# Kernel tuning notes

Hardware: AMD Instinct MI355X
Metric: run time of the kernel (lower is better)

The kernel has to match this reference:

```python
import jax, jax.numpy as jnp
import numpy as np

NUM_HEADS = 5
TEMP = 0.3
NEG_FILL = -1e-7  # note: NOT -inf; masked entries still contribute ~exp(0) to softmax, faithful to torch code


def setup_inputs() -> dict:
    key = jax.random.key(0)
    k1, k2, k3, k4, k5 = jax.random.split(key, 5)
    B, N, F_IN, F_OUT = 8, 1024, 320, 320
    h = jax.random.normal(k1, (B, N, F_IN), dtype=jnp.float32)
    Wqk = jax.random.normal(k2, (F_IN, 2 * F_IN), dtype=jnp.float32) * (1.0 / np.sqrt(F_IN))
    bqk = jax.random.normal(k3, (2 * F_IN,), dtype=jnp.float32) * 0.01
    weight = jax.random.normal(k4, (F_IN, F_OUT), dtype=jnp.float32) * (1.0 / np.sqrt(F_OUT))
    bias = jax.random.normal(k5, (F_OUT,), dtype=jnp.float32) * 0.01
    return {"h": h, "Wqk": Wqk, "bqk": bqk, "weight": weight, "bias": bias}


def reference(h, Wqk, bqk, weight, bias):
    B, N, F = h.shape
    H = NUM_HEADS
    D = F // H
    # linear -> [b, n, 2F]; einops 'b n (h d qk)' => reshape (b, n, h, d, 2)
    qk = (h @ Wqk + bqk).reshape(B, N, H, D, 2)
    q = jnp.transpose(qk[..., 0], (0, 2, 1, 3))  # b h n d
    k = jnp.transpose(qk[..., 1], (0, 2, 1, 3))  # b h n d
    scale = D ** -0.5
    dots = jnp.einsum('bhqd,bhkd->bhqk', q, k) * scale  # b h n n
    at = dots.sum(axis=1)  # b n n  (sum over heads)
    # sort-based threshold: keep values >= descending-sorted value at index N//6
    thr = jax.lax.top_k(at, N // 6 + 1)[0][..., -1]  # b n
    adj = jnp.where(at < thr[:, :, None], jnp.asarray(NEG_FILL, at.dtype), at)
    attn = jax.nn.softmax(adj / TEMP, axis=2)  # b n n
    out_feature = jnp.einsum('bij,bjd->bid', attn, h)  # values = raw input h
    return out_feature @ weight + bias
```

## Files before the change

### kernel.cpp

```cpp
#include <hip/hip_runtime.h>
#include <hip/hip_fp16.h>


typedef __attribute__((ext_vector_type(8))) _Float16 half8;
typedef __attribute__((ext_vector_type(4))) float f32x4;

__device__ __forceinline__ void stage_tile(const __half* g, __half* lds,
                                           int nrow16, int ld, int wave, int lane) {
    const int r = lane >> 2;
    const int c = ((lane & 3) ^ ((lane >> 3) & 3)) * 8;
    for (int i = wave; i < nrow16; i += 4) {
        const __half* src = g + (long)(i * 16 + r) * ld + c;
        __builtin_amdgcn_global_load_lds(
            (const __attribute__((address_space(1))) unsigned int*)src,
            (__attribute__((address_space(3))) unsigned int*)(lds + i * 512),
            16, 0, 0);
    }
}

template <int WM, int WN, int EPI>
__global__ __launch_bounds__(256) void gemm_nt(
    const __half* __restrict__ A, const __half* __restrict__ B,
    void* __restrict__ C, void* __restrict__ C2,
    const float* __restrict__ bias,
    int K, int lda, int ldb, int ldc,
    long sA, long sB, long sC, float alpha)
{
    constexpr int BM = WM * 64;
    constexpr int BN = WN * 64;
    constexpr int BUF = BM * 32 + BN * 32;
    __shared__ __half smem[2 * BUF];

    const int tid  = threadIdx.x;
    const int lane = tid & 63;
    const int wave = tid >> 6;
    const int wm   = wave / WN;
    const int wn   = wave % WN;
    const int bz   = blockIdx.z;

    const __half* Ab = A + bz * sA + (long)blockIdx.y * BM * lda;
    const __half* Bb = B + bz * sB + (long)blockIdx.x * BN * ldb;

    f32x4 acc[4][4];
    #pragma unroll
    for (int i = 0; i < 4; ++i)
        #pragma unroll
        for (int j = 0; j < 4; ++j) acc[i][j] = (f32x4){0.f, 0.f, 0.f, 0.f};

    const int lrow = lane & 15;
    const int quad = lane >> 4;
    const int swz = (quad ^ ((lrow >> 1) & 3)) * 8;

    const int nIter = K >> 5;

    stage_tile(Ab, smem, BM / 16, lda, wave, lane);
    stage_tile(Bb, smem + BM * 32, BN / 16, ldb, wave, lane);

    for (int it = 0; it < nIter; ++it) {
        __syncthreads();

        if (it + 1 < nIter) {
            __half* nb = smem + ((it + 1) & 1) * BUF;
            const int k1 = (it + 1) << 5;
            stage_tile(Ab + k1, nb, BM / 16, lda, wave, lane);
            stage_tile(Bb + k1, nb + BM * 32, BN / 16, ldb, wave, lane);
        }

        const __half* buf = smem + (it & 1) * BUF;
        const __half* pA = buf + (wm * 64 + lrow) * 32 + swz;
        const __half* pB = buf + BM * 32 + (wn * 64 + lrow) * 32 + swz;
        half8 ah[4], bh[4];
        #pragma unroll
        for (int mt = 0; mt < 4; ++mt) ah[mt] = *(const half8*)(pA + mt * 512);
        #pragma unroll
        for (int nt = 0; nt < 4; ++nt) bh[nt] = *(const half8*)(pB + nt * 512);
        #pragma unroll
        for (int mt = 0; mt < 4; ++mt)
            #pragma unroll
            for (int nt = 0; nt < 4; ++nt)
                acc[mt][nt] = __builtin_amdgcn_mfma_f32_16x16x32_f16(
                    ah[mt], bh[nt], acc[mt][nt], 0, 0, 0);
    }

    const int row_base = blockIdx.y * BM + wm * 64;
    const int col_base = blockIdx.x * BN + wn * 64;
    #pragma unroll
    for (int mt = 0; mt < 4; ++mt)
        #pragma unroll
        for (int nt = 0; nt < 4; ++nt)
            #pragma unroll
            for (int r = 0; r < 4; ++r) {
                const int row = row_base + mt * 16 + quad * 4 + r;
                const int col = col_base + nt * 16 + lrow;
                const float v = acc[mt][nt][r];
                if (EPI == 1) {
                    const float val = v + bias[col];
                    const long idx = (long)row * 320 + (col >> 1);
                    if (col & 1) ((__half*)C2)[idx] = __float2half(val);
                    else         ((__half*)C)[idx]  = __float2half(val);
                } else if (EPI == 2) {
                    ((__half*)C)[(long)row * ldc + col] = __float2half(v);
                } else if (EPI == 3) {
                    ((float*)C)[bz * sC + (long)row * ldc + col] = v + bias[col];
                } else {
                    ((__half*)C)[bz * sC + (long)row * ldc + col] =
                        __float2half(alpha * v);
                }
            }
}

__global__ __launch_bounds__(256) void prep_all(
    const float* __restrict__ h, ushort4* __restrict__ h16,
    const float* __restrict__ Wqk, __half* __restrict__ WqkT,
    const float* __restrict__ weight, __half* __restrict__ wTp)
{
    const int bx = blockIdx.x;
    if (bx < 2560) {
        const int i = bx * 256 + threadIdx.x;
        const float4 v = ((const float4*)h)[i];
        ushort4 o;
        o.x = __half_as_ushort(__float2half(v.x));
        o.y = __half_as_ushort(__float2half(v.y));
        o.z = __half_as_ushort(__float2half(v.z));
        o.w = __half_as_ushort(__float2half(v.w));
        h16[i] = o;
        return;
    }
    __shared__ float t[32][33];
    const float* src;
    __half* dst;
    int ldS, ldT, c0, r0;
    if (bx < 2760) {
        const int b = bx - 2560;
        src = Wqk; dst = WqkT; ldS = 640; ldT = 320;
        c0 = (b % 20) * 32; r0 = (b / 20) * 32;
    } else {
        const int b = bx - 2760;
        src = weight; dst = wTp; ldS = 320; ldT = 320;
        c0 = (b % 10) * 32; r0 = (b / 10) * 32;
    }
    const int lx = threadIdx.x & 31, ly = threadIdx.x >> 5;
    #pragma unroll
    for (int i = 0; i < 4; ++i)
        t[ly + 8 * i][lx] = src[(long)(r0 + ly + 8 * i) * ldS + c0 + lx];
    __syncthreads();
    #pragma unroll
    for (int i = 0; i < 4; ++i)
        dst[(long)(c0 + ly + 8 * i) * ldT + r0 + lx] = __float2half(t[lx][ly + 8 * i]);
}

__global__ __launch_bounds__(256) void topk_softmax(const __half* __restrict__ at,
                                                    __half* __restrict__ attn)
{
    __shared__ int hist[4][256];
    const int lane = threadIdx.x & 63;
    const int wave = threadIdx.x >> 6;
    const long row = (long)blockIdx.x * 4 + wave;

    unsigned short vs[16];
    {
        const uint4* p = (const uint4*)(at + row * 1024 + lane * 16);
        *(uint4*)&vs[0] = p[0];
        *(uint4*)&vs[8] = p[1];
    }

    unsigned key[16];
    #pragma unroll
    for (int i = 0; i < 16; ++i) {
        const unsigned u = vs[i];
        key[i] = (u & 0x8000u) ? ((~u) & 0xFFFFu) : (u | 0x8000u);
    }

    unsigned prefix = 0, pmask = 0;
    int kk = 171;

    #pragma unroll
    for (int pass = 0; pass < 2; ++pass) {
        const int shift = 8 - 8 * pass;
        *(int4*)&hist[wave][lane * 4] = make_int4(0, 0, 0, 0);
        __syncthreads();
        #pragma unroll
        for (int i = 0; i < 16; ++i) {
            if ((key[i] & pmask) == prefix)
                atomicAdd(&hist[wave][(key[i] >> shift) & 255], 1);
        }
        __syncthreads();
        const int4 hh = *(const int4*)&hist[wave][lane * 4];
        const int s = hh.x + hh.y + hh.z + hh.w;
        int suf = s;
        #pragma unroll
        for (int off = 1; off < 64; off <<= 1) {
            const int o = __shfl_down(suf, off);
            if (lane + off < 64) suf += o;
        }
        const int cgt3 = suf - s;
        const int cgt2 = cgt3 + hh.w;
        const int cgt1 = cgt2 + hh.z;
        const int cgt0 = cgt1 + hh.y;
        int pick = 0x7FFFFFFF;
        if (cgt3 < kk && kk <= cgt3 + hh.w) pick = ((4 * lane + 3) << 16) | (kk - cgt3);
        if (cgt2 < kk && kk <= cgt2 + hh.z) pick = ((4 * lane + 2) << 16) | (kk - cgt2);
        if (cgt1 < kk && kk <= cgt1 + hh.y) pick = ((4 * lane + 1) << 16) | (kk - cgt1);
        if (cgt0 < kk && kk <= cgt0 + hh.x) pick = ((4 * lane + 0) << 16) | (kk - cgt0);
        #pragma unroll
        for (int off = 32; off > 0; off >>= 1) pick = min(pick, __shfl_xor(pick, off));
        const unsigned digit = (unsigned)(pick >> 16);
        kk = pick & 0xFFFF;
        prefix |= digit << shift;
        pmask  |= 0xFFu << shift;
        if (pass == 0) __syncthreads();
    }

    const unsigned short tu = (prefix & 0x8000u) ? (unsigned short)(prefix & 0x7FFFu)
                                                 : (unsigned short)((~prefix) & 0xFFFFu);
    const float thr = __half2float(__ushort_as_half(tu));

    float lg[16];
    float mx = -3.4e38f;
    #pragma unroll
    for (int i = 0; i < 16; ++i) {
        const float v = __half2float(__ushort_as_half(vs[i]));
        const float a = (v < thr) ? -1e-7f : v;
        lg[i] = a * (1.0f / 0.3f);
        mx = fmaxf(mx, lg[i]);
    }
    #pragma unroll
    for (int off = 32; off > 0; off >>= 1) mx = fmaxf(mx, __shfl_xor(mx, off));

    float e[16];
    float sum = 0.f;
    #pragma unroll
    for (int i = 0; i < 16; ++i) { e[i] = __expf(lg[i] - mx); sum += e[i]; }
    #pragma unroll
    for (int off = 32; off > 0; off >>= 1) sum += __shfl_xor(sum, off);
    const float inv = 1.0f / sum;

    unsigned short os[16];
    #pragma unroll
    for (int i = 0; i < 16; ++i) os[i] = __half_as_ushort(__float2half(e[i] * inv));
    uint4* q = (uint4*)(attn + row * 1024 + lane * 16);
    q[0] = *(const uint4*)&os[0];
    q[1] = *(const uint4*)&os[8];
}

extern "C" void kernel_launch(void* const* d_in, const int* in_sizes, int n_in,
                              void* d_out, int out_size, void* d_ws, size_t ws_size,
                              hipStream_t stream) {
    (void)in_sizes; (void)n_in; (void)out_size; (void)ws_size;

    const float* h      = (const float*)d_in[0];
    const float* Wqk    = (const float*)d_in[1];
    const float* bqk    = (const float*)d_in[2];
    const float* weight = (const float*)d_in[3];
    const float* bias   = (const float*)d_in[4];
    float* out = (float*)d_out;

    char* p = (char*)d_ws;
    __half* at   = (__half*)p; p += 8388608L * 2;
    __half* attn = (__half*)p; p += 8388608L * 2;
    __half* h16  = (__half*)p; p += 2621440L * 2;
    __half* Q    = (__half*)p; p += 2621440L * 2;
    __half* Kb   = (__half*)p; p += 2621440L * 2;
    __half* WqkT = (__half*)p; p += 640L * 320 * 2;
    __half* wTp  = (__half*)p; p += 384L * 320 * 2;
    __half* hWT  = (__half*)p; p += 384L * 8192 * 2;

    prep_all<<<2860, 256, 0, stream>>>(h, (ushort4*)h16, Wqk, WqkT, weight, wTp);

    gemm_nt<2, 2, 2><<<dim3(64, 3, 1), 256, 0, stream>>>(
        wTp, h16, hWT, nullptr, nullptr,
        320, 320, 320, 8192, 0, 0, 0, 1.0f);

    gemm_nt<4, 1, 1><<<dim3(10, 32, 1), 256, 0, stream>>>(
        h16, WqkT, Q, Kb, bqk,
        320, 320, 320, 0, 0, 0, 0, 1.0f);

    gemm_nt<2, 2, 4><<<dim3(8, 8, 8), 256, 0, stream>>>(
        Q, Kb, at, nullptr, nullptr,
        320, 320, 320, 1024, 327680, 327680, 1048576, 0.125f);

    topk_softmax<<<2048, 256, 0, stream>>>(at, attn);

    gemm_nt<4, 1, 3><<<dim3(5, 4, 8), 256, 0, stream>>>(
        attn, hWT, out, nullptr, bias,
        1024, 1024, 8192, 320, 1048576, 1024, 327680, 1.0f);
}
```

Baseline: 146.0 us.

## Fuse QK^T, top-k softmax, and attn@hW into one per-row-block kernel

```diff
diff --git a/kernel.cpp b/kernel.cpp
--- a/kernel.cpp
+++ b/kernel.cpp
@@ -4,6 +4,8 @@
 
 typedef __attribute__((ext_vector_type(8))) _Float16 half8;
 typedef __attribute__((ext_vector_type(4))) float f32x4;
+
+#define ATP 1056
 
 __device__ __forceinline__ void stage_tile(const __half* g, __half* lds,
                                            int nrow16, int ld, int wave, int lane) {
@@ -18,28 +20,21 @@
     }
 }
 
-template <int WM, int WN, int EPI>
-__global__ __launch_bounds__(256) void gemm_nt(
+template <int EPI>
+__device__ __forceinline__ void gemm_body(
     const __half* __restrict__ A, const __half* __restrict__ B,
-    void* __restrict__ C, void* __restrict__ C2,
-    const float* __restrict__ bias,
-    int K, int lda, int ldb, int ldc,
-    long sA, long sB, long sC, float alpha)
+    void* __restrict__ C, void* __restrict__ C2, const float* __restrict__ bias,
+    int lda, int ldb, int ldc, int bx, int by, __half* smem)
 {
-    constexpr int BM = WM * 64;
-    constexpr int BN = WN * 64;
-    constexpr int BUF = BM * 32 + BN * 32;
-    __shared__ __half smem[2 * BUF];
-
+    constexpr int BUF = 8192;
     const int tid  = threadIdx.x;
     const int lane = tid & 63;
     const int wave = tid >> 6;
-    const int wm   = wave / WN;
-    const int wn   = wave % WN;
-    const int bz   = blockIdx.z;
-
-    const __half* Ab = A + bz * sA + (long)blockIdx.y * BM * lda;
-    const __half* Bb = B + bz * sB + (long)blockIdx.x * BN * ldb;
+    const int wm   = wave >> 1;
+    const int wn   = wave & 1;
+
+    const __half* Ab = A + (long)by * 128 * lda;
+    const __half* Bb = B + (long)bx * 128 * ldb;
 
     f32x4 acc[4][4];
     #pragma unroll
@@ -51,24 +46,19 @@
     const int quad = lane >> 4;
     const int swz = (quad ^ ((lrow >> 1) & 3)) * 8;
 
-    const int nIter = K >> 5;
-
-    stage_tile(Ab, smem, BM / 16, lda, wave, lane);
-    stage_tile(Bb, smem + BM * 32, BN / 16, ldb, wave, lane);
-
-    for (int it = 0; it < nIter; ++it) {
+    stage_tile(Ab, smem, 8, lda, wave, lane);
+    stage_tile(Bb, smem + 4096, 8, ldb, wave, lane);
+
+    for (int it = 0; it < 10; ++it) {
         __syncthreads();
-
-        if (it + 1 < nIter) {
+        if (it + 1 < 10) {
             __half* nb = smem + ((it + 1) & 1) * BUF;
-            const int k1 = (it + 1) << 5;
-            stage_tile(Ab + k1, nb, BM / 16, lda, wave, lane);
-            stage_tile(Bb + k1, nb + BM * 32, BN / 16, ldb, wave, lane);
-        }
-
+            stage_tile(Ab + (it + 1) * 32, nb, 8, lda, wave, lane);
+            stage_tile(Bb + (it + 1) * 32, nb + 4096, 8, ldb, wave, lane);
+        }
         const __half* buf = smem + (it & 1) * BUF;
         const __half* pA = buf + (wm * 64 + lrow) * 32 + swz;
-        const __half* pB = buf + BM * 32 + (wn * 64 + lrow) * 32 + swz;
+        const __half* pB = buf + 4096 + (wn * 64 + lrow) * 32 + swz;
         half8 ah[4], bh[4];
         #pragma unroll
         for (int mt = 0; mt < 4; ++mt) ah[mt] = *(const half8*)(pA + mt * 512);
@@ -82,8 +72,8 @@
                     ah[mt], bh[nt], acc[mt][nt], 0, 0, 0);
     }
 
-    const int row_base = blockIdx.y * BM + wm * 64;
-    const int col_base = blockIdx.x * BN + wn * 64;
+    const int row_base = by * 128 + wm * 64;
+    const int col_base = bx * 128 + wn * 64;
     #pragma unroll
     for (int mt = 0; mt < 4; ++mt)
         #pragma unroll
@@ -98,15 +88,28 @@
                     const long idx = (long)row * 320 + (col >> 1);
                     if (col & 1) ((__half*)C2)[idx] = __float2half(val);
                     else         ((__half*)C)[idx]  = __float2half(val);
-                } else if (EPI == 2) {
+                } else {
                     ((__half*)C)[(long)row * ldc + col] = __float2half(v);
-                } else if (EPI == 3) {
-                    ((float*)C)[bz * sC + (long)row * ldc + col] = v + bias[col];
-                } else {
-                    ((__half*)C)[bz * sC + (long)row * ldc + col] =
-                        __float2half(alpha * v);
                 }
             }
+}
+
+__global__ __launch_bounds__(256) void g1_combined(
+    const __half* __restrict__ h16, const __half* __restrict__ wTp,
+    const __half* __restrict__ WqkT, __half* __restrict__ hWT,
+    __half* __restrict__ Q, __half* __restrict__ Kb,
+    const float* __restrict__ bqk)
+{
+    __shared__ __half smem[2 * 8192];
+    const int bx = blockIdx.x;
+    if (bx < 192) {
+        gemm_body<2>(wTp, h16, hWT, nullptr, nullptr,
+                     320, 320, 8192, bx % 64, bx / 64, smem);
+    } else {
+        const int b = bx - 192;
+        gemm_body<1>(h16, WqkT, Q, Kb, bqk,
+                     320, 320, 320, b % 5, b / 5, smem);
+    }
 }
 
 __global__ __launch_bounds__(256) void prep_all(
@@ -149,98 +152,208 @@
         dst[(long)(c0 + ly + 8 * i) * ldT + r0 + lx] = __float2half(t[lx][ly + 8 * i]);
 }
 
-__global__ __launch_bounds__(256) void topk_softmax(const __half* __restrict__ at,
-                                                    __half* __restrict__ attn)
+__global__ __launch_bounds__(256) void attn_fused(
+    const __half* __restrict__ Q, const __half* __restrict__ Kmat,
+    const __half* __restrict__ hWT, const float* __restrict__ bias,
+    float* __restrict__ out)
 {
+    __shared__ __half sAT[32 * ATP];
+    __shared__ __half sStg[2 * 10240];
     __shared__ int hist[4][256];
-    const int lane = threadIdx.x & 63;
-    const int wave = threadIdx.x >> 6;
-    const long row = (long)blockIdx.x * 4 + wave;
-
-    unsigned short vs[16];
-    {
-        const uint4* p = (const uint4*)(at + row * 1024 + lane * 16);
-        *(uint4*)&vs[0] = p[0];
-        *(uint4*)&vs[8] = p[1];
-    }
-
-    unsigned key[16];
-    #pragma unroll
-    for (int i = 0; i < 16; ++i) {
-        const unsigned u = vs[i];
-        key[i] = (u & 0x8000u) ? ((~u) & 0xFFFFu) : (u | 0x8000u);
-    }
-
-    unsigned prefix = 0, pmask = 0;
-    int kk = 171;
-
-    #pragma unroll
-    for (int pass = 0; pass < 2; ++pass) {
-        const int shift = 8 - 8 * pass;
-        *(int4*)&hist[wave][lane * 4] = make_int4(0, 0, 0, 0);
+
+    const int tid  = threadIdx.x;
+    const int lane = tid & 63;
+    const int wave = tid >> 6;
+    const int lrow = lane & 15;
+    const int quad = lane >> 4;
+    const int swz  = (quad ^ ((lrow >> 1) & 3)) * 8;
+
+    const int batch = blockIdx.x >> 5;
+    const int r0    = (blockIdx.x & 31) * 32;
+    const __half* Qb = Q    + ((long)batch * 1024 + r0) * 320;
+    const __half* Kb = Kmat + (long)batch * 1024 * 320;
+    const __half* Wb = hWT  + (long)batch * 1024;
+    float* outB = out + ((long)batch * 1024 + r0) * 320;
+
+    for (int cc = 0; cc < 4; ++cc) {
+        const __half* Kcc = Kb + (long)(cc * 256) * 320;
+        stage_tile(Qb, sStg, 2, 320, wave, lane);
+        stage_tile(Kcc, sStg + 1024, 16, 320, wave, lane);
+
+        f32x4 acc[2][4];
+        #pragma unroll
+        for (int i = 0; i < 2; ++i)
+            #pragma unroll
+            for (int j = 0; j < 4; ++j) acc[i][j] = (f32x4){0.f, 0.f, 0.f, 0.f};
+
+        for (int it = 0; it < 10; ++it) {
+            __syncthreads();
+            if (it + 1 < 10) {
+                __half* nb = sStg + ((it + 1) & 1) * 10240;
+                stage_tile(Qb + (it + 1) * 32, nb, 2, 320, wave, lane);
+                stage_tile(Kcc + (it + 1) * 32, nb + 1024, 16, 320, wave, lane);
+            }
+            const __half* buf = sStg + (it & 1) * 10240;
+            half8 qf[2], kf[4];
+            #pragma unroll
+            for (int mt = 0; mt < 2; ++mt)
+                qf[mt] = *(const half8*)(buf + (mt * 16 + lrow) * 32 + swz);
+            #pragma unroll
+            for (int nt = 0; nt < 4; ++nt)
+                kf[nt] = *(const half8*)(buf + 1024 + (wave * 64 + nt * 16 + lrow) * 32 + swz);
+            #pragma unroll
+            for (int mt = 0; mt < 2; ++mt)
+                #pragma unroll
+                for (int nt = 0; nt < 4; ++nt)
+                    acc[mt][nt] = __builtin_amdgcn_mfma_f32_16x16x32_f16(
+                        qf[mt], kf[nt], acc[mt][nt], 0, 0, 0);
+        }
+        #pragma unroll
+        for (int mt = 0; mt < 2; ++mt)
+            #pragma unroll
+            for (int nt = 0; nt < 4; ++nt)
+                #pragma unroll
+                for (int rg = 0; rg < 4; ++rg) {
+                    const int row = mt * 16 + quad * 4 + rg;
+                    const int col = cc * 256 + wave * 64 + nt * 16 + lrow;
+                    const int slot = ((col >> 3) & 3) ^ ((row >> 1) & 3);
+                    sAT[row * ATP + (col >> 5) * 32 + slot * 8 + (col & 7)] =
+                        __float2half(0.125f * acc[mt][nt][rg]);
+                }
+    }
+    __syncthreads();
+
+    for (int rr = 0; rr < 8; ++rr) {
+        const int row = wave * 8 + rr;
+        const int rsw = (row >> 1) & 3;
+        unsigned short vs[16];
+        #pragma unroll
+        for (int j = 0; j < 2; ++j) {
+            const int g = lane * 2 + j;
+            const int addr = row * ATP + (g >> 2) * 32 + ((g & 3) ^ rsw) * 8;
+            *(uint4*)&vs[8 * j] = *(const uint4*)&sAT[addr];
+        }
+
+        unsigned key[16];
+        #pragma unroll
+        for (int i = 0; i < 16; ++i) {
+            const unsigned u = vs[i];
+            key[i] = (u & 0x8000u) ? ((~u) & 0xFFFFu) : (u | 0x8000u);
+        }
+
+        unsigned prefix = 0, pmask = 0;
+        int kk = 171;
+        #pragma unroll
+        for (int pass = 0; pass < 2; ++pass) {
+            const int shift = 8 - 8 * pass;
+            *(int4*)&hist[wave][lane * 4] = make_int4(0, 0, 0, 0);
+            __syncthreads();
+            #pragma unroll
+            for (int i = 0; i < 16; ++i) {
+                if ((key[i] & pmask) == prefix)
+                    atomicAdd(&hist[wave][(key[i] >> shift) & 255], 1);
+            }
+            __syncthreads();
+            const int4 hh = *(const int4*)&hist[wave][lane * 4];
+            const int s = hh.x + hh.y + hh.z + hh.w;
+            int suf = s;
+            #pragma unroll
+            for (int off = 1; off < 64; off <<= 1) {
+                const int o = __shfl_down(suf, off);
+                if (lane + off < 64) suf += o;
+            }
+            const int cgt3 = suf - s;
+            const int cgt2 = cgt3 + hh.w;
+            const int cgt1 = cgt2 + hh.z;
+            const int cgt0 = cgt1 + hh.y;
+            int pick = 0x7FFFFFFF;
+            if (cgt3 < kk && kk <= cgt3 + hh.w) pick = ((4 * lane + 3) << 16) | (kk - cgt3);
+            if (cgt2 < kk && kk <= cgt2 + hh.z) pick = ((4 * lane + 2) << 16) | (kk - cgt2);
+            if (cgt1 < kk && kk <= cgt1 + hh.y) pick = ((4 * lane + 1) << 16) | (kk - cgt1);
+            if (cgt0 < kk && kk <= cgt0 + hh.x) pick = ((4 * lane + 0) << 16) | (kk - cgt0);
+            #pragma unroll
+            for (int off = 32; off > 0; off >>= 1) pick = min(pick, __shfl_xor(pick, off));
+            kk = pick & 0xFFFF;
+            prefix |= ((unsigned)(pick >> 16)) << shift;
+            pmask  |= 0xFFu << shift;
+            if (pass == 0) __syncthreads();
+        }
+
+        const unsigned short tu = (prefix & 0x8000u) ? (unsigned short)(prefix & 0x7FFFu)
+                                                     : (unsigned short)((~prefix) & 0xFFFFu);
+        const float thr = __half2float(__ushort_as_half(tu));
+
+        float lg[16];
+        float mx = -3.4e38f;
+        #pragma unroll
+        for (int i = 0; i < 16; ++i) {
+            const float v = __half2float(__ushort_as_half(vs[i]));
+            const float a = (v < thr) ? -1e-7f : v;
+            lg[i] = a * (1.0f / 0.3f);
+            mx = fmaxf(mx, lg[i]);
+        }
+        #pragma unroll
+        for (int off = 32; off > 0; off >>= 1) mx = fmaxf(mx, __shfl_xor(mx, off));
+
+        float e[16];
+        float sum = 0.f;
+        #pragma unroll
+        for (int i = 0; i < 16; ++i) { e[i] = __expf(lg[i] - mx); sum += e[i]; }
+        #pragma unroll
+        for (int off = 32; off > 0; off >>= 1) sum += __shfl_xor(sum, off);
+        const float inv = 1.0f / sum;
+
+        unsigned short os[16];
+        #pragma unroll
+        for (int i = 0; i < 16; ++i) os[i] = __half_as_ushort(__float2half(e[i] * inv));
+        #pragma unroll
+        for (int j = 0; j < 2; ++j) {
+            const int g = lane * 2 + j;
+            const int addr = row * ATP + (g >> 2) * 32 + ((g & 3) ^ rsw) * 8;
+            *(uint4*)&sAT[addr] = *(const uint4*)&os[8 * j];
+        }
+    }
+    __syncthreads();
+
+    f32x4 acc3[2][5];
+    #pragma unroll
+    for (int i = 0; i < 2; ++i)
+        #pragma unroll
+        for (int j = 0; j < 5; ++j) acc3[i][j] = (f32x4){0.f, 0.f, 0.f, 0.f};
+
+    stage_tile(Wb, sStg, 20, 8192, wave, lane);
+    for (int it = 0; it < 32; ++it) {
         __syncthreads();
-        #pragma unroll
-        for (int i = 0; i < 16; ++i) {
-            if ((key[i] & pmask) == prefix)
-                atomicAdd(&hist[wave][(key[i] >> shift) & 255], 1);
-        }
-        __syncthreads();
-        const int4 hh = *(const int4*)&hist[wave][lane * 4];
-        const int s = hh.x + hh.y + hh.z + hh.w;
-        int suf = s;
-        #pragma unroll
-        for (int off = 1; off < 64; off <<= 1) {
-            const int o = __shfl_down(suf, off);
-            if (lane + off < 64) suf += o;
-        }
-        const int cgt3 = suf - s;
-        const int cgt2 = cgt3 + hh.w;
-        const int cgt1 = cgt2 + hh.z;
-        const int cgt0 = cgt1 + hh.y;
-        int pick = 0x7FFFFFFF;
-        if (cgt3 < kk && kk <= cgt3 + hh.w) pick = ((4 * lane + 3) << 16) | (kk - cgt3);
-        if (cgt2 < kk && kk <= cgt2 + hh.z) pick = ((4 * lane + 2) << 16) | (kk - cgt2);
-        if (cgt1 < kk && kk <= cgt1 + hh.y) pick = ((4 * lane + 1) << 16) | (kk - cgt1);
-        if (cgt0 < kk && kk <= cgt0 + hh.x) pick = ((4 * lane + 0) << 16) | (kk - cgt0);
-        #pragma unroll
-        for (int off = 32; off > 0; off >>= 1) pick = min(pick, __shfl_xor(pick, off));
-        const unsigned digit = (unsigned)(pick >> 16);
-        kk = pick & 0xFFFF;
-        prefix |= digit << shift;
-        pmask  |= 0xFFu << shift;
-        if (pass == 0) __syncthreads();
-    }
-
-    const unsigned short tu = (prefix & 0x8000u) ? (unsigned short)(prefix & 0x7FFFu)
-                                                 : (unsigned short)((~prefix) & 0xFFFFu);
-    const float thr = __half2float(__ushort_as_half(tu));
-
-    float lg[16];
-    float mx = -3.4e38f;
-    #pragma unroll
-    for (int i = 0; i < 16; ++i) {
-        const float v = __half2float(__ushort_as_half(vs[i]));
-        const float a = (v < thr) ? -1e-7f : v;
-        lg[i] = a * (1.0f / 0.3f);
-        mx = fmaxf(mx, lg[i]);
-    }
-    #pragma unroll
-    for (int off = 32; off > 0; off >>= 1) mx = fmaxf(mx, __shfl_xor(mx, off));
-
-    float e[16];
-    float sum = 0.f;
-    #pragma unroll
-    for (int i = 0; i < 16; ++i) { e[i] = __expf(lg[i] - mx); sum += e[i]; }
-    #pragma unroll
-    for (int off = 32; off > 0; off >>= 1) sum += __shfl_xor(sum, off);
-    const float inv = 1.0f / sum;
-
-    unsigned short os[16];
-    #pragma unroll
-    for (int i = 0; i < 16; ++i) os[i] = __half_as_ushort(__float2half(e[i] * inv));
-    uint4* q = (uint4*)(attn + row * 1024 + lane * 16);
-    q[0] = *(const uint4*)&os[0];
-    q[1] = *(const uint4*)&os[8];
+        if (it + 1 < 32)
+            stage_tile(Wb + (it + 1) * 32, sStg + ((it + 1) & 1) * 10240,
+                       20, 8192, wave, lane);
+        const __half* buf = sStg + (it & 1) * 10240;
+        const int k0 = it * 32;
+        half8 af[2], bf[5];
+        #pragma unroll
+        for (int mt = 0; mt < 2; ++mt)
+            af[mt] = *(const half8*)(sAT + (mt * 16 + lrow) * ATP + k0 + swz);
+        #pragma unroll
+        for (int j = 0; j < 5; ++j)
+            bf[j] = *(const half8*)(buf + ((wave * 5 + j) * 16 + lrow) * 32 + swz);
+        #pragma unroll
+        for (int mt = 0; mt < 2; ++mt)
+            #pragma unroll
+            for (int j = 0; j < 5; ++j)
+                acc3[mt][j] = __builtin_amdgcn_mfma_f32_16x16x32_f16(
+                    af[mt], bf[j], acc3[mt][j], 0, 0, 0);
+    }
+
+    #pragma unroll
+    for (int mt = 0; mt < 2; ++mt)
+        #pragma unroll
+        for (int j = 0; j < 5; ++j)
+            #pragma unroll
+            for (int rg = 0; rg < 4; ++rg) {
+                const int row = mt * 16 + quad * 4 + rg;
+                const int col = wave * 80 + j * 16 + lrow;
+                outB[(long)row * 320 + col] = acc3[mt][j][rg] + bias[col];
+            }
 }
 
 extern "C" void kernel_launch(void* const* d_in, const int* in_sizes, int n_in,
@@ -256,8 +369,6 @@
     float* out = (float*)d_out;
 
     char* p = (char*)d_ws;
-    __half* at   = (__half*)p; p += 8388608L * 2;
-    __half* attn = (__half*)p; p += 8388608L * 2;
     __half* h16  = (__half*)p; p += 2621440L * 2;
     __half* Q    = (__half*)p; p += 2621440L * 2;
     __half* Kb   = (__half*)p; p += 2621440L * 2;
@@ -267,21 +378,7 @@
 
     prep_all<<<2860, 256, 0, stream>>>(h, (ushort4*)h16, Wqk, WqkT, weight, wTp);
 
-    gemm_nt<2, 2, 2><<<dim3(64, 3, 1), 256, 0, stream>>>(
-        wTp, h16, hWT, nullptr, nullptr,
-        320, 320, 320, 8192, 0, 0, 0, 1.0f);
-
-    gemm_nt<4, 1, 1><<<dim3(10, 32, 1), 256, 0, stream>>>(
-        h16, WqkT, Q, Kb, bqk,
-        320, 320, 320, 0, 0, 0, 0, 1.0f);
-
-    gemm_nt<2, 2, 4><<<dim3(8, 8, 8), 256, 0, stream>>>(
-        Q, Kb, at, nullptr, nullptr,
-        320, 320, 320, 1024, 327680, 327680, 1048576, 0.125f);
-
-    topk_softmax<<<2048, 256, 0, stream>>>(at, attn);
-
-    gemm_nt<4, 1, 3><<<dim3(5, 4, 8), 256, 0, stream>>>(
-        attn, hWT, out, nullptr, bias,
-        1024, 1024, 8192, 320, 1048576, 1024, 327680, 1.0f);
-}
+    g1_combined<<<512, 256, 0, stream>>>(h16, wTp, WqkT, hWT, Q, Kb, bqk);
+
+    attn_fused<<<256, 256, 0, stream>>>(Q, Kb, hWT, bias, out);
+}
```

Result: slower. 157.2 us (+7.7%).
